# Performance work log

Hardware: AMD Instinct MI355X
Metric: run time of the kernel (lower is better)

The kernel has to match this reference:

```python
import jax, jax.numpy as jnp
import numpy as np

B, T, C = 4, 2048, 768
N_HEADS = 16
HEAD_DIM = C // N_HEADS  # 48
ROPE_BASE = 10000.0


def setup_inputs() -> dict:
    key = jax.random.key(0)
    ks = jax.random.split(key, 6)
    s = 0.02
    return {
        "hidden_states": jax.random.normal(ks[0], (B, T, C), dtype=jnp.float32),
        "attention_mask": jnp.ones((B, T), dtype=jnp.float32),
        "Wq": jax.random.normal(ks[1], (C, C), dtype=jnp.float32) * s,
        "bq": jnp.zeros((C,), dtype=jnp.float32),
        "Wk": jax.random.normal(ks[2], (C, C), dtype=jnp.float32) * s,
        "bk": jnp.zeros((C,), dtype=jnp.float32),
        "Wv": jax.random.normal(ks[3], (C, C), dtype=jnp.float32) * s,
        "bv": jnp.zeros((C,), dtype=jnp.float32),
        "Wo": jax.random.normal(ks[4], (C, C), dtype=jnp.float32) * s,
        "bo": jnp.zeros((C,), dtype=jnp.float32),
    }


def _rotate_half(x):
    x1, x2 = jnp.split(x, 2, axis=-1)
    return jnp.concatenate([-x2, x1], axis=-1)


def reference(hidden_states, attention_mask, Wq, bq, Wk, bk, Wv, bv, Wo, bo):
    b, t, c = hidden_states.shape
    h, d = N_HEADS, c // N_HEADS

    def split_heads(x):  # [b,t,c] -> [b,h,t,d]
        return x.reshape(b, t, h, d).transpose(0, 2, 1, 3)

    q = split_heads(hidden_states @ Wq.T + bq)
    k = split_heads(hidden_states @ Wk.T + bk)
    v = split_heads(hidden_states @ Wv.T + bv)

    # rotary embedding: cos/sin [t, d]
    pos = jnp.arange(t, dtype=jnp.float32)
    inv_freq = 1.0 / (ROPE_BASE ** (jnp.arange(0, d, 2, dtype=jnp.float32) / d))
    freqs = pos[:, None] * inv_freq[None, :]          # [t, d/2]
    emb = jnp.concatenate([freqs, freqs], axis=-1)    # [t, d]
    cos, sin = jnp.cos(emb), jnp.sin(emb)
    q = q * cos + _rotate_half(q) * sin
    k = k * cos + _rotate_half(k) * sin

    scores = jnp.einsum('bhqd,bhkd->bhqk', q, k) / jnp.sqrt(jnp.asarray(d, q.dtype))
    # additive padding mask: (1 - mask) * -10000, broadcast [b,1,1,t]
    scores = scores + (1.0 - attention_mask)[:, None, None, :] * -10000.0
    # causal mask with -inf
    causal = jnp.tril(jnp.ones((t, t), dtype=bool))
    scores = jnp.where(causal[None, None], scores, -jnp.inf)

    probs = jax.nn.softmax(scores, axis=-1)
    ctx = jnp.einsum('bhqk,bhkd->bhqd', probs, v)
    ctx = ctx.transpose(0, 2, 1, 3).reshape(b, t, c)
    return ctx @ Wo.T + bo
```

## Files before the change

kernel.cpp:

```cpp
#include <hip/hip_runtime.h>
#include <hip/hip_bf16.h>
#include <math.h>

#define BB 4
#define TT 2048
#define CC 768
#define NHD 16
#define HD 48
#define NQT 32

typedef __hip_bfloat16 bf16;
typedef __attribute__((ext_vector_type(8))) short short8;
typedef __attribute__((ext_vector_type(4))) float floatx4;

__device__ __forceinline__ unsigned short f2bf(float x) {
    bf16 h = __float2bfloat16(x);
    return *(unsigned short*)&h;
}
__device__ __forceinline__ float bfu2f(unsigned short u) {
    return __uint_as_float(((unsigned)u) << 16);
}

__device__ __forceinline__ void gl_lds16(const void* g, void* s) {
    __builtin_amdgcn_global_load_lds((const __attribute__((address_space(1))) void*)g,
                                     (__attribute__((address_space(3))) void*)s, 16, 0, 0);
}

__device__ __forceinline__ unsigned int pk_bf2(float a, float b) {
    unsigned int ua = __float_as_uint(a) + 0x8000u;
    unsigned int ub = __float_as_uint(b) + 0x8000u;
    return __builtin_amdgcn_perm(ub, ua, 0x07060302);
}

__global__ __launch_bounds__(256) void cast_hs(const float* __restrict__ src,
                                               unsigned short* __restrict__ dst) {
    int i = (blockIdx.x * 256 + threadIdx.x) * 4;
    float4 v = *(const float4*)(src + i);
    ushort4 p;
    p.x = f2bf(v.x); p.y = f2bf(v.y); p.z = f2bf(v.z); p.w = f2bf(v.w);
    *(ushort4*)(dst + i) = p;
}

__global__ __launch_bounds__(256) void cast_w4(const float* __restrict__ s0, const float* __restrict__ s1,
                                               const float* __restrict__ s2, const float* __restrict__ s3,
                                               unsigned short* __restrict__ d0, unsigned short* __restrict__ d1,
                                               unsigned short* __restrict__ d2, unsigned short* __restrict__ d3) {
    const float* s; unsigned short* d;
    switch (blockIdx.y) {
        case 0: s = s0; d = d0; break;
        case 1: s = s1; d = d1; break;
        case 2: s = s2; d = d2; break;
        default: s = s3; d = d3; break;
    }
    int i = (blockIdx.x * 256 + threadIdx.x) * 4;
    float4 v = *(const float4*)(s + i);
    ushort4 p;
    p.x = f2bf(v.x); p.y = f2bf(v.y); p.z = f2bf(v.z); p.w = f2bf(v.w);
    *(ushort4*)(d + i) = p;
}

__global__ __launch_bounds__(256) void rope_table(float2* __restrict__ tab) {
    int idx = blockIdx.x * 256 + threadIdx.x;
    int t = idx / 24, p = idx % 24;
    float inv_freq = powf(10000.0f, -((float)(2 * p) / (float)HD));
    float ang = (float)t * inv_freq;
    float sn, cs;
    sincosf(ang, &sn, &cs);
    tab[idx] = make_float2(cs, sn);
}

template <int MODE>
__global__ __launch_bounds__(256) void gemm_mfma(const unsigned short* __restrict__ A,
                                                 const unsigned short* __restrict__ Bw,
                                                 const float* __restrict__ b0p,
                                                 const float* __restrict__ b1p,
                                                 const float* __restrict__ b2p,
                                                 void* __restrict__ out0,
                                                 void* __restrict__ out1,
                                                 void* __restrict__ out2) {
    __shared__ __align__(16) unsigned short As[128][64];
    __shared__ __align__(16) unsigned short Bs[128][64];
    const int tid = threadIdx.x;
    const int w = tid >> 6, lane = tid & 63;
    const int quad = lane >> 4, ln = lane & 15;
    const int wr = w >> 1, wc = w & 1;

    const int NXB = (MODE == 1) ? 18 : 6;
    const int bx = blockIdx.x;
    const int xcd = bx & 7, slot = bx >> 3;
    const int n0 = (slot % NXB) * 128;
    const int m0 = ((slot / NXB) * 8 + xcd) * 128;

    const int srow = lane >> 3;
    const int ssw = ((lane & 7) ^ srow) * 8;
    const unsigned short* agp[4];
    const unsigned short* bgp[4];
    void* asl[4];
    void* bsl[4];
#pragma unroll
    for (int i = 0; i < 4; ++i) {
        const int R = i * 32 + w * 8;
        agp[i] = A + (size_t)(m0 + R + srow) * CC + ssw;
        bgp[i] = Bw + (size_t)(n0 + R + srow) * CC + ssw;
        asl[i] = &As[R][0];
        bsl[i] = &Bs[R][0];
    }

    floatx4 acc[4][4];
#pragma unroll
    for (int mi = 0; mi < 4; ++mi)
#pragma unroll
        for (int ni = 0; ni < 4; ++ni) acc[mi][ni] = (floatx4){0.f, 0.f, 0.f, 0.f};

    const int ps0 = (quad ^ (ln & 7)) * 8;

    for (int k0 = 0; k0 < CC; k0 += 64) {
        __syncthreads();
#pragma unroll
        for (int i = 0; i < 4; ++i) {
            gl_lds16(agp[i] + k0, asl[i]);
            gl_lds16(bgp[i] + k0, bsl[i]);
        }
        __syncthreads();
#pragma unroll
        for (int kh = 0; kh < 2; ++kh) {
            const int ps = ps0 ^ (kh * 32);
            short8 af[4], bfr[4];
#pragma unroll
            for (int mi = 0; mi < 4; ++mi)
                af[mi] = *(const short8*)&As[wr * 64 + mi * 16 + ln][ps];
#pragma unroll
            for (int ni = 0; ni < 4; ++ni)
                bfr[ni] = *(const short8*)&Bs[wc * 64 + ni * 16 + ln][ps];
#pragma unroll
            for (int mi = 0; mi < 4; ++mi)
#pragma unroll
                for (int ni = 0; ni < 4; ++ni)
                    acc[mi][ni] = __builtin_amdgcn_mfma_f32_16x16x32_bf16(af[mi], bfr[ni], acc[mi][ni], 0, 0, 0);
        }
    }

    if (MODE == 0) {
        float* outf = (float*)out0;
        float bv[4];
#pragma unroll
        for (int ni = 0; ni < 4; ++ni) bv[ni] = b0p[n0 + wc * 64 + ni * 16 + ln];
#pragma unroll
        for (int mi = 0; mi < 4; ++mi)
#pragma unroll
            for (int r = 0; r < 4; ++r) {
                size_t row = m0 + wr * 64 + mi * 16 + quad * 4 + r;
#pragma unroll
                for (int ni = 0; ni < 4; ++ni)
                    outf[row * CC + n0 + wc * 64 + ni * 16 + ln] = acc[mi][ni][r] + bv[ni];
            }
    } else {
        const int seg = n0 / CC;
        const int nl0 = n0 - seg * CC;
        const float* bp = (seg == 0) ? b0p : (seg == 1) ? b1p : b2p;
        float bv[4];
#pragma unroll
        for (int ni = 0; ni < 4; ++ni) bv[ni] = bp[nl0 + wc * 64 + ni * 16 + ln];

        if (seg < 2) {
            unsigned short* outb = (unsigned short*)(seg == 0 ? out0 : out1);
#pragma unroll
            for (int mi = 0; mi < 4; ++mi)
#pragma unroll
                for (int r = 0; r < 4; ++r) {
                    size_t row = m0 + wr * 64 + mi * 16 + quad * 4 + r;
#pragma unroll
                    for (int ni = 0; ni < 4; ++ni)
                        outb[row * CC + nl0 + wc * 64 + ni * 16 + ln] = f2bf(acc[mi][ni][r] + bv[ni]);
                }
        } else {
            unsigned short* outb = (unsigned short*)out2;
            const int b = m0 >> 11;
#pragma unroll
            for (int ni = 0; ni < 4; ++ni) {
                int col = nl0 + wc * 64 + ni * 16 + ln;
                int h = col / HD, d = col % HD;
                size_t base = (size_t)((b * NHD + h) * HD + d) * TT;
#pragma unroll
                for (int mi = 0; mi < 4; ++mi) {
                    int t = (m0 & 2047) + wr * 64 + mi * 16 + quad * 4;
                    ushort4 pk;
                    pk.x = f2bf(acc[mi][ni][0] + bv[ni]);
                    pk.y = f2bf(acc[mi][ni][1] + bv[ni]);
                    pk.z = f2bf(acc[mi][ni][2] + bv[ni]);
                    pk.w = f2bf(acc[mi][ni][3] + bv[ni]);
                    *(ushort4*)(outb + base + t) = pk;
                }
            }
        }
    }
}

__global__ __launch_bounds__(256) void rope_bf(unsigned short* __restrict__ q,
                                               unsigned short* __restrict__ k,
                                               const float2* __restrict__ tab) {
    int idx = blockIdx.x * blockDim.x + threadIdx.x;
    const int HALF = HD / 2;
    int p = idx % HALF;
    int rest = idx / HALF;
    int h = rest % NHD;
    int n = rest / NHD;
    int t = n % TT;
    const float QSC = 0.14433756729740643f * 1.4426950408889634f;
    float2 cssn = tab[t * HALF + p];
    float cs = cssn.x, sn = cssn.y;
    size_t base = (size_t)n * CC + h * HD + p;
    float x1 = bfu2f(q[base]), x2 = bfu2f(q[base + HALF]);
    q[base] = f2bf((x1 * cs - x2 * sn) * QSC);
    q[base + HALF] = f2bf((x2 * cs + x1 * sn) * QSC);
    x1 = bfu2f(k[base]); x2 = bfu2f(k[base + HALF]);
    k[base] = f2bf(x1 * cs - x2 * sn);
    k[base + HALF] = f2bf(x2 * cs + x1 * sn);
}

__global__ __launch_bounds__(256) void attn_kernel(const unsigned short* __restrict__ qb,
                                                   const unsigned short* __restrict__ kb,
                                                   const unsigned short* __restrict__ vt,
                                                   const float* __restrict__ amask,
                                                   unsigned short* __restrict__ ctx) {
    const int bx = blockIdx.x;
    const int xcd = bx & 7;
    const int rem = bx >> 3;
    const int pair = rem & 15;
    const int j = ((rem >> 4) << 3) | xcd;
    const int b = j >> 4, h = j & 15;
    const int tid = threadIdx.x;
    const int w = tid >> 6, lane = tid & 63;
    const int g = lane >> 4, ln = lane & 15;

    __shared__ __align__(16) unsigned short Qs[64][72];
    __shared__ __align__(16) unsigned short Ks[64][72];
    __shared__ __align__(16) unsigned short Vs[64][72];
    __shared__ __align__(16) unsigned short Pw[4][16][72];
    __shared__ __align__(16) float l_s[4][16];

    {
        short8 z8 = {0, 0, 0, 0, 0, 0, 0, 0};
        short8 o8 = {0x3F80, 0, 0, 0, 0, 0, 0, 0};
        short8 ones8 = {0x3F80, 0x3F80, 0x3F80, 0x3F80, 0x3F80, 0x3F80, 0x3F80, 0x3F80};
        if (tid < 128) {
            int r = tid >> 1, half = tid & 1;
            *(short8*)&Qs[r][48 + half * 8] = half ? z8 : o8;
            int t2 = tid;
            *(short8*)&Ks[t2 >> 1][48 + (t2 & 1) * 8] = z8;
        } else if (tid < 128 + 144) {
            int t3 = tid - 128;
            int r = 48 + t3 / 9, cseg = t3 % 9;
            *(short8*)&Vs[r][cseg * 8] = (r == 48) ? ones8 : z8;
        }
    }

    const int ck1 = tid + 256;
    const int rK0 = tid / 6, sK0 = tid % 6;
    const int rK1 = ck1 / 6, sK1 = ck1 % 6;
    const int rV0 = tid >> 3, sV0 = tid & 7;
    const int rV1 = ck1 >> 3, sV1 = ck1 & 7;
    const unsigned short* kbase0 = kb + (size_t)(b * TT + rK0) * CC + h * HD + sK0 * 8;
    const unsigned short* kbase1 = kb + (size_t)(b * TT + rK1) * CC + h * HD + sK1 * 8;
    const unsigned short* vbase0 = vt + (size_t)((b * NHD + h) * HD + rV0) * TT + sV0 * 8;
    const unsigned short* vbase1 = vt + (size_t)((b * NHD + h) * HD + rV1) * TT + sV1 * 8;
    const float* mbase = amask + b * TT + (tid & 63);
    const float MBS = -10000.0f * 1.4426950408889634f;

    for (int rep = 0; rep < 2; ++rep) {
        const int qt = rep ? (NQT - 1 - pair) : pair;
        const int q0 = qt * 64;
        __syncthreads();
        *(short8*)&Qs[rK0][sK0 * 8] =
            *(const short8*)(qb + (size_t)(b * TT + q0 + rK0) * CC + h * HD + sK0 * 8);
        if (tid < 128)
            *(short8*)&Qs[rK1][sK1 * 8] =
                *(const short8*)(qb + (size_t)(b * TT + q0 + rK1) * CC + h * HD + sK1 * 8);

        const unsigned short* kp0 = kbase0;
        const unsigned short* kp1 = kbase1;
        const unsigned short* vp0 = vbase0;
        const unsigned short* vp1 = vbase1;
        const float* mp = mbase;
        short8 kr0, kr1, vr0, vr1;
        float mr = 1.0f;
        kr0 = *(const short8*)kp0;
        vr0 = *(const short8*)vp0;
        if (tid < 128) { kr1 = *(const short8*)kp1; vr1 = *(const short8*)vp1; }
        if (tid < 64) mr = *mp;
        __syncthreads();

        short8 aq0 = *(const short8*)&Qs[w * 16 + ln][g * 8];
        short8 aq1 = *(const short8*)&Qs[w * 16 + ln][32 + g * 8];
        const int q_lane = q0 + w * 16 + ln;

        floatx4 o0 = {0.f, 0.f, 0.f, 0.f}, o1 = o0, o2 = o0, o3 = o0;

        for (int kt = 0; kt <= qt; ++kt) {
            __syncthreads();
            *(short8*)&Ks[rK0][sK0 * 8] = kr0;
            *(short8*)&Vs[rV0][sV0 * 8] = vr0;
            if (tid < 128) {
                *(short8*)&Ks[rK1][sK1 * 8] = kr1;
                *(short8*)&Vs[rV1][sV1 * 8] = vr1;
            }
            if (tid < 64) Ks[tid][48] = f2bf((1.0f - mr) * MBS);
            __syncthreads();

            if (kt < qt) {
                kp0 += (size_t)64 * CC; kr0 = *(const short8*)kp0;
                vp0 += 64;              vr0 = *(const short8*)vp0;
                if (tid < 128) {
                    kp1 += (size_t)64 * CC; kr1 = *(const short8*)kp1;
                    vp1 += 64;              vr1 = *(const short8*)vp1;
                }
                if (tid < 64) { mp += 64; mr = *mp; }
            }

            const int k0 = kt * 64;
            floatx4 sc[4];
#pragma unroll
            for (int c = 0; c < 4; ++c) {
                short8 kf0 = *(const short8*)&Ks[c * 16 + ln][g * 8];
                short8 kf1 = *(const short8*)&Ks[c * 16 + ln][32 + g * 8];
                floatx4 z = {0.f, 0.f, 0.f, 0.f};
                z = __builtin_amdgcn_mfma_f32_16x16x32_bf16(kf0, aq0, z, 0, 0, 0);
                z = __builtin_amdgcn_mfma_f32_16x16x32_bf16(kf1, aq1, z, 0, 0, 0);
                sc[c] = z;
            }

            const bool diag = (kt == qt);
#pragma unroll
            for (int c = 0; c < 4; ++c) {
                float pv[4];
#pragma unroll
                for (int r = 0; r < 4; ++r) {
                    float e = __builtin_amdgcn_exp2f(sc[c][r]);
                    if (diag && (k0 + c * 16 + g * 4 + r > q_lane)) e = 0.f;
                    pv[r] = e;
                }
                uint2 pk;
                pk.x = pk_bf2(pv[0], pv[1]);
                pk.y = pk_bf2(pv[2], pv[3]);
                *(uint2*)&Pw[w][ln][c * 16 + g * 4] = pk;
            }
            short8 pa0 = *(const short8*)&Pw[w][ln][g * 8];
            short8 pa1 = *(const short8*)&Pw[w][ln][32 + g * 8];
#pragma unroll
            for (int n = 0; n < 4; ++n) {
                short8 vb0 = *(const short8*)&Vs[n * 16 + ln][g * 8];
                short8 vb1 = *(const short8*)&Vs[n * 16 + ln][32 + g * 8];
                floatx4 acc = (n == 0) ? o0 : (n == 1) ? o1 : (n == 2) ? o2 : o3;
                acc = __builtin_amdgcn_mfma_f32_16x16x32_bf16(pa0, vb0, acc, 0, 0, 0);
                acc = __builtin_amdgcn_mfma_f32_16x16x32_bf16(pa1, vb1, acc, 0, 0, 0);
                if (n == 0) o0 = acc; else if (n == 1) o1 = acc; else if (n == 2) o2 = acc; else o3 = acc;
            }
        }

        if (ln == 0) *(floatx4*)&l_s[w][g * 4] = o3;
        floatx4 l4 = *(const floatx4*)&l_s[w][g * 4];
#pragma unroll
        for (int r = 0; r < 4; ++r) {
            float inv_l = 1.0f / l4[r];
            int t = q0 + w * 16 + g * 4 + r;
            unsigned short* dst = ctx + (size_t)(b * TT + t) * CC + h * HD;
            dst[ln] = f2bf(o0[r] * inv_l);
            dst[16 + ln] = f2bf(o1[r] * inv_l);
            dst[32 + ln] = f2bf(o2[r] * inv_l);
        }
    }
}

extern "C" void kernel_launch(void* const* d_in, const int* in_sizes, int n_in,
                              void* d_out, int out_size, void* d_ws, size_t ws_size,
                              hipStream_t stream) {
    const float* hs = (const float*)d_in[0];
    const float* amask = (const float*)d_in[1];
    const float* Wq = (const float*)d_in[2];
    const float* bq = (const float*)d_in[3];
    const float* Wk = (const float*)d_in[4];
    const float* bk = (const float*)d_in[5];
    const float* Wv = (const float*)d_in[6];
    const float* bv = (const float*)d_in[7];
    const float* Wo = (const float*)d_in[8];
    const float* bo = (const float*)d_in[9];

    const size_t NELEM = (size_t)BB * TT * CC;
    const size_t WELEM = (size_t)CC * CC;
    unsigned short* hb  = (unsigned short*)d_ws;
    unsigned short* qbuf = hb + NELEM;
    unsigned short* kbuf = qbuf + NELEM;
    unsigned short* vtb = kbuf + NELEM;
    unsigned short* ctxb = vtb + NELEM;
    unsigned short* wqb = ctxb + NELEM;
    unsigned short* wkb = wqb + WELEM;
    unsigned short* wvb = wkb + WELEM;
    unsigned short* wob = wvb + WELEM;
    float2* ropetab = (float2*)(wob + WELEM);

    cast_hs<<<NELEM / 1024, 256, 0, stream>>>(hs, hb);
    dim3 wgrid(WELEM / 1024, 4);
    cast_w4<<<wgrid, 256, 0, stream>>>(Wq, Wk, Wv, Wo, wqb, wkb, wvb, wob);
    rope_table<<<(TT * (HD / 2)) / 256, 256, 0, stream>>>(ropetab);

    gemm_mfma<1><<<18 * 64, 256, 0, stream>>>(hb, wqb, bq, bk, bv, qbuf, kbuf, vtb);

    int rope_total = BB * TT * NHD * (HD / 2);
    rope_bf<<<rope_total / 256, 256, 0, stream>>>(qbuf, kbuf, ropetab);

    attn_kernel<<<1024, 256, 0, stream>>>(qbuf, kbuf, vtb, amask, ctxb);

    gemm_mfma<0><<<6 * 64, 256, 0, stream>>>(ctxb, wob, bo, nullptr, nullptr,
                                             (float*)d_out, nullptr, nullptr);
}
```

Before: 234.6 us.

## Split attention to one Q tile per block, load Q/V straight to registers, vectorize RoPE

Each attention block now handles a single query tile, with tiles interleaved light and heavy, instead of a pair of complementary tiles. The grid doubles to 2048 blocks and occupancy is raised with a launch-bounds hint. Q fragments and V fragments are read directly from global memory into MFMA operand registers, which removes the Q and V shared-memory tiles and their staging. A constant ones vector supplies the row-sum column. RoPE now processes 8 elements per thread with 16-byte vector loads and stores. The risks are more uncoalesced per-lane global V reads inside the loop with no prefetch, and per-block load imbalance across the causal tiles.

New measurement: 394.3 us. 68.0% more time.

```diff
diff --git a/kernel.cpp b/kernel.cpp
--- a/kernel.cpp
+++ b/kernel.cpp
@@ -201,173 +201,171 @@
                                                const float2* __restrict__ tab) {
     int idx = blockIdx.x * blockDim.x + threadIdx.x;
     const int HALF = HD / 2;
-    int p = idx % HALF;
-    int rest = idx / HALF;
+    int p8 = idx % 3;
+    int rest = idx / 3;
     int h = rest % NHD;
     int n = rest / NHD;
-    int t = n % TT;
+    int t = n & (TT - 1);
     const float QSC = 0.14433756729740643f * 1.4426950408889634f;
-    float2 cssn = tab[t * HALF + p];
-    float cs = cssn.x, sn = cssn.y;
-    size_t base = (size_t)n * CC + h * HD + p;
-    float x1 = bfu2f(q[base]), x2 = bfu2f(q[base + HALF]);
-    q[base] = f2bf((x1 * cs - x2 * sn) * QSC);
-    q[base + HALF] = f2bf((x2 * cs + x1 * sn) * QSC);
-    x1 = bfu2f(k[base]); x2 = bfu2f(k[base + HALF]);
-    k[base] = f2bf(x1 * cs - x2 * sn);
-    k[base + HALF] = f2bf(x2 * cs + x1 * sn);
-}
-
-__global__ __launch_bounds__(256) void attn_kernel(const unsigned short* __restrict__ qb,
-                                                   const unsigned short* __restrict__ kb,
-                                                   const unsigned short* __restrict__ vt,
-                                                   const float* __restrict__ amask,
-                                                   unsigned short* __restrict__ ctx) {
+    size_t base = (size_t)n * CC + h * HD + p8 * 8;
+    const float2* tp = tab + t * HALF + p8 * 8;
+
+    short8 q1 = *(const short8*)(q + base);
+    short8 q2 = *(const short8*)(q + base + HALF);
+    short8 k1 = *(const short8*)(k + base);
+    short8 k2 = *(const short8*)(k + base + HALF);
+    short8 r1, r2, s1, s2;
+#pragma unroll
+    for (int jj = 0; jj < 8; ++jj) {
+        float2 cssn = tp[jj];
+        float cs = cssn.x, sn = cssn.y;
+        float a = bfu2f((unsigned short)q1[jj]), bb = bfu2f((unsigned short)q2[jj]);
+        r1[jj] = (short)f2bf((a * cs - bb * sn) * QSC);
+        r2[jj] = (short)f2bf((bb * cs + a * sn) * QSC);
+        float c2 = bfu2f((unsigned short)k1[jj]), d2 = bfu2f((unsigned short)k2[jj]);
+        s1[jj] = (short)f2bf(c2 * cs - d2 * sn);
+        s2[jj] = (short)f2bf(d2 * cs + c2 * sn);
+    }
+    *(short8*)(q + base) = r1;
+    *(short8*)(q + base + HALF) = r2;
+    *(short8*)(k + base) = s1;
+    *(short8*)(k + base + HALF) = s2;
+}
+
+__global__ __launch_bounds__(256, 8) void attn_kernel(const unsigned short* __restrict__ qb,
+                                                      const unsigned short* __restrict__ kb,
+                                                      const unsigned short* __restrict__ vt,
+                                                      const float* __restrict__ amask,
+                                                      unsigned short* __restrict__ ctx) {
     const int bx = blockIdx.x;
     const int xcd = bx & 7;
     const int rem = bx >> 3;
-    const int pair = rem & 15;
-    const int j = ((rem >> 4) << 3) | xcd;
+    const int u = rem & 31;
+    const int qt = (u & 1) ? (31 - (u >> 1)) : (u >> 1);
+    const int j = ((rem >> 5) << 3) | xcd;
     const int b = j >> 4, h = j & 15;
     const int tid = threadIdx.x;
     const int w = tid >> 6, lane = tid & 63;
     const int g = lane >> 4, ln = lane & 15;
 
-    __shared__ __align__(16) unsigned short Qs[64][72];
     __shared__ __align__(16) unsigned short Ks[64][72];
-    __shared__ __align__(16) unsigned short Vs[64][72];
     __shared__ __align__(16) unsigned short Pw[4][16][72];
     __shared__ __align__(16) float l_s[4][16];
 
-    {
-        short8 z8 = {0, 0, 0, 0, 0, 0, 0, 0};
-        short8 o8 = {0x3F80, 0, 0, 0, 0, 0, 0, 0};
-        short8 ones8 = {0x3F80, 0x3F80, 0x3F80, 0x3F80, 0x3F80, 0x3F80, 0x3F80, 0x3F80};
-        if (tid < 128) {
-            int r = tid >> 1, half = tid & 1;
-            *(short8*)&Qs[r][48 + half * 8] = half ? z8 : o8;
-            int t2 = tid;
-            *(short8*)&Ks[t2 >> 1][48 + (t2 & 1) * 8] = z8;
-        } else if (tid < 128 + 144) {
-            int t3 = tid - 128;
-            int r = 48 + t3 / 9, cseg = t3 % 9;
-            *(short8*)&Vs[r][cseg * 8] = (r == 48) ? ones8 : z8;
-        }
+    const short8 z8 = {0, 0, 0, 0, 0, 0, 0, 0};
+    const short8 ones8 = {0x3F80, 0x3F80, 0x3F80, 0x3F80, 0x3F80, 0x3F80, 0x3F80, 0x3F80};
+
+    if (tid < 128) {
+        int r = tid >> 1, half = tid & 1;
+        *(short8*)&Ks[r][48 + half * 8] = z8;
     }
 
     const int ck1 = tid + 256;
     const int rK0 = tid / 6, sK0 = tid % 6;
     const int rK1 = ck1 / 6, sK1 = ck1 % 6;
-    const int rV0 = tid >> 3, sV0 = tid & 7;
-    const int rV1 = ck1 >> 3, sV1 = ck1 & 7;
-    const unsigned short* kbase0 = kb + (size_t)(b * TT + rK0) * CC + h * HD + sK0 * 8;
-    const unsigned short* kbase1 = kb + (size_t)(b * TT + rK1) * CC + h * HD + sK1 * 8;
-    const unsigned short* vbase0 = vt + (size_t)((b * NHD + h) * HD + rV0) * TT + sV0 * 8;
-    const unsigned short* vbase1 = vt + (size_t)((b * NHD + h) * HD + rV1) * TT + sV1 * 8;
-    const float* mbase = amask + b * TT + (tid & 63);
+    const unsigned short* kp0 = kb + (size_t)(b * TT + rK0) * CC + h * HD + sK0 * 8;
+    const unsigned short* kp1 = kb + (size_t)(b * TT + rK1) * CC + h * HD + sK1 * 8;
+    const float* mp = amask + b * TT + (tid & 63);
     const float MBS = -10000.0f * 1.4426950408889634f;
 
-    for (int rep = 0; rep < 2; ++rep) {
-        const int qt = rep ? (NQT - 1 - pair) : pair;
-        const int q0 = qt * 64;
+    const unsigned short* vp0 = vt + ((size_t)((b * NHD + h) * HD) + 0 * 16 + ln) * TT + g * 8;
+    const unsigned short* vp1 = vt + ((size_t)((b * NHD + h) * HD) + 1 * 16 + ln) * TT + g * 8;
+    const unsigned short* vp2 = vt + ((size_t)((b * NHD + h) * HD) + 2 * 16 + ln) * TT + g * 8;
+    const short8 vone = (ln == 0) ? ones8 : z8;
+
+    const int q0 = qt * 64;
+
+    const unsigned short* qrow = qb + (size_t)(b * TT + q0 + w * 16 + ln) * CC + h * HD;
+    short8 aq0 = *(const short8*)(qrow + g * 8);
+    short8 aq1;
+    if (g < 2) {
+        aq1 = *(const short8*)(qrow + 32 + g * 8);
+    } else {
+        aq1 = z8;
+        if (g == 2) aq1[0] = (short)0x3F80;
+    }
+
+    short8 kr0, kr1;
+    float mr = 1.0f;
+    kr0 = *(const short8*)kp0;
+    if (tid < 128) kr1 = *(const short8*)kp1;
+    if (tid < 64) mr = *mp;
+
+    const int q_lane = q0 + w * 16 + ln;
+    floatx4 o0 = {0.f, 0.f, 0.f, 0.f}, o1 = o0, o2 = o0, o3 = o0;
+
+    for (int kt = 0; kt <= qt; ++kt) {
         __syncthreads();
-        *(short8*)&Qs[rK0][sK0 * 8] =
-            *(const short8*)(qb + (size_t)(b * TT + q0 + rK0) * CC + h * HD + sK0 * 8);
-        if (tid < 128)
-            *(short8*)&Qs[rK1][sK1 * 8] =
-                *(const short8*)(qb + (size_t)(b * TT + q0 + rK1) * CC + h * HD + sK1 * 8);
-
-        const unsigned short* kp0 = kbase0;
-        const unsigned short* kp1 = kbase1;
-        const unsigned short* vp0 = vbase0;
-        const unsigned short* vp1 = vbase1;
-        const float* mp = mbase;
-        short8 kr0, kr1, vr0, vr1;
-        float mr = 1.0f;
-        kr0 = *(const short8*)kp0;
-        vr0 = *(const short8*)vp0;
-        if (tid < 128) { kr1 = *(const short8*)kp1; vr1 = *(const short8*)vp1; }
-        if (tid < 64) mr = *mp;
+        *(short8*)&Ks[rK0][sK0 * 8] = kr0;
+        if (tid < 128) *(short8*)&Ks[rK1][sK1 * 8] = kr1;
+        if (tid < 64) Ks[tid][48] = f2bf((1.0f - mr) * MBS);
         __syncthreads();
 
-        short8 aq0 = *(const short8*)&Qs[w * 16 + ln][g * 8];
-        short8 aq1 = *(const short8*)&Qs[w * 16 + ln][32 + g * 8];
-        const int q_lane = q0 + w * 16 + ln;
-
-        floatx4 o0 = {0.f, 0.f, 0.f, 0.f}, o1 = o0, o2 = o0, o3 = o0;
-
-        for (int kt = 0; kt <= qt; ++kt) {
-            __syncthreads();
-            *(short8*)&Ks[rK0][sK0 * 8] = kr0;
-            *(short8*)&Vs[rV0][sV0 * 8] = vr0;
-            if (tid < 128) {
-                *(short8*)&Ks[rK1][sK1 * 8] = kr1;
-                *(short8*)&Vs[rV1][sV1 * 8] = vr1;
+        if (kt < qt) {
+            kp0 += (size_t)64 * CC; kr0 = *(const short8*)kp0;
+            if (tid < 128) { kp1 += (size_t)64 * CC; kr1 = *(const short8*)kp1; }
+            if (tid < 64) { mp += 64; mr = *mp; }
+        }
+
+        const int k0 = kt * 64;
+        floatx4 sc[4];
+#pragma unroll
+        for (int c = 0; c < 4; ++c) {
+            short8 kf0 = *(const short8*)&Ks[c * 16 + ln][g * 8];
+            short8 kf1 = *(const short8*)&Ks[c * 16 + ln][32 + g * 8];
+            floatx4 z = {0.f, 0.f, 0.f, 0.f};
+            z = __builtin_amdgcn_mfma_f32_16x16x32_bf16(kf0, aq0, z, 0, 0, 0);
+            z = __builtin_amdgcn_mfma_f32_16x16x32_bf16(kf1, aq1, z, 0, 0, 0);
+            sc[c] = z;
+        }
+
+        const bool diag = (kt == qt);
+#pragma unroll
+        for (int c = 0; c < 4; ++c) {
+            float pv[4];
+#pragma unroll
+            for (int r = 0; r < 4; ++r) {
+                float e = __builtin_amdgcn_exp2f(sc[c][r]);
+                if (diag && (k0 + c * 16 + g * 4 + r > q_lane)) e = 0.f;
+                pv[r] = e;
             }
-            if (tid < 64) Ks[tid][48] = f2bf((1.0f - mr) * MBS);
-            __syncthreads();
-
-            if (kt < qt) {
-                kp0 += (size_t)64 * CC; kr0 = *(const short8*)kp0;
-                vp0 += 64;              vr0 = *(const short8*)vp0;
-                if (tid < 128) {
-                    kp1 += (size_t)64 * CC; kr1 = *(const short8*)kp1;
-                    vp1 += 64;              vr1 = *(const short8*)vp1;
-                }
-                if (tid < 64) { mp += 64; mr = *mp; }
-            }
-
-            const int k0 = kt * 64;
-            floatx4 sc[4];
-#pragma unroll
-            for (int c = 0; c < 4; ++c) {
-                short8 kf0 = *(const short8*)&Ks[c * 16 + ln][g * 8];
-                short8 kf1 = *(const short8*)&Ks[c * 16 + ln][32 + g * 8];
-                floatx4 z = {0.f, 0.f, 0.f, 0.f};
-                z = __builtin_amdgcn_mfma_f32_16x16x32_bf16(kf0, aq0, z, 0, 0, 0);
-                z = __builtin_amdgcn_mfma_f32_16x16x32_bf16(kf1, aq1, z, 0, 0, 0);
-                sc[c] = z;
-            }
-
-            const bool diag = (kt == qt);
-#pragma unroll
-            for (int c = 0; c < 4; ++c) {
-                float pv[4];
-#pragma unroll
-                for (int r = 0; r < 4; ++r) {
-                    float e = __builtin_amdgcn_exp2f(sc[c][r]);
-                    if (diag && (k0 + c * 16 + g * 4 + r > q_lane)) e = 0.f;
-                    pv[r] = e;
-                }
-                uint2 pk;
-                pk.x = pk_bf2(pv[0], pv[1]);
-                pk.y = pk_bf2(pv[2], pv[3]);
-                *(uint2*)&Pw[w][ln][c * 16 + g * 4] = pk;
-            }
-            short8 pa0 = *(const short8*)&Pw[w][ln][g * 8];
-            short8 pa1 = *(const short8*)&Pw[w][ln][32 + g * 8];
-#pragma unroll
-            for (int n = 0; n < 4; ++n) {
-                short8 vb0 = *(const short8*)&Vs[n * 16 + ln][g * 8];
-                short8 vb1 = *(const short8*)&Vs[n * 16 + ln][32 + g * 8];
-                floatx4 acc = (n == 0) ? o0 : (n == 1) ? o1 : (n == 2) ? o2 : o3;
-                acc = __builtin_amdgcn_mfma_f32_16x16x32_bf16(pa0, vb0, acc, 0, 0, 0);
-                acc = __builtin_amdgcn_mfma_f32_16x16x32_bf16(pa1, vb1, acc, 0, 0, 0);
-                if (n == 0) o0 = acc; else if (n == 1) o1 = acc; else if (n == 2) o2 = acc; else o3 = acc;
-            }
-        }
-
-        if (ln == 0) *(floatx4*)&l_s[w][g * 4] = o3;
-        floatx4 l4 = *(const floatx4*)&l_s[w][g * 4];
-#pragma unroll
-        for (int r = 0; r < 4; ++r) {
-            float inv_l = 1.0f / l4[r];
-            int t = q0 + w * 16 + g * 4 + r;
-            unsigned short* dst = ctx + (size_t)(b * TT + t) * CC + h * HD;
-            dst[ln] = f2bf(o0[r] * inv_l);
-            dst[16 + ln] = f2bf(o1[r] * inv_l);
-            dst[32 + ln] = f2bf(o2[r] * inv_l);
-        }
+            uint2 pk;
+            pk.x = pk_bf2(pv[0], pv[1]);
+            pk.y = pk_bf2(pv[2], pv[3]);
+            *(uint2*)&Pw[w][ln][c * 16 + g * 4] = pk;
+        }
+
+        short8 v00 = *(const short8*)vp0;
+        short8 v01 = *(const short8*)(vp0 + 32);
+        short8 v10 = *(const short8*)vp1;
+        short8 v11 = *(const short8*)(vp1 + 32);
+        short8 v20 = *(const short8*)vp2;
+        short8 v21 = *(const short8*)(vp2 + 32);
+        vp0 += 64; vp1 += 64; vp2 += 64;
+
+        short8 pa0 = *(const short8*)&Pw[w][ln][g * 8];
+        short8 pa1 = *(const short8*)&Pw[w][ln][32 + g * 8];
+
+        o0 = __builtin_amdgcn_mfma_f32_16x16x32_bf16(pa0, v00, o0, 0, 0, 0);
+        o0 = __builtin_amdgcn_mfma_f32_16x16x32_bf16(pa1, v01, o0, 0, 0, 0);
+        o1 = __builtin_amdgcn_mfma_f32_16x16x32_bf16(pa0, v10, o1, 0, 0, 0);
+        o1 = __builtin_amdgcn_mfma_f32_16x16x32_bf16(pa1, v11, o1, 0, 0, 0);
+        o2 = __builtin_amdgcn_mfma_f32_16x16x32_bf16(pa0, v20, o2, 0, 0, 0);
+        o2 = __builtin_amdgcn_mfma_f32_16x16x32_bf16(pa1, v21, o2, 0, 0, 0);
+        o3 = __builtin_amdgcn_mfma_f32_16x16x32_bf16(pa0, vone, o3, 0, 0, 0);
+        o3 = __builtin_amdgcn_mfma_f32_16x16x32_bf16(pa1, vone, o3, 0, 0, 0);
+    }
+
+    if (ln == 0) *(floatx4*)&l_s[w][g * 4] = o3;
+    floatx4 l4 = *(const floatx4*)&l_s[w][g * 4];
+#pragma unroll
+    for (int r = 0; r < 4; ++r) {
+        float inv_l = 1.0f / l4[r];
+        int t = q0 + w * 16 + g * 4 + r;
+        unsigned short* dst = ctx + (size_t)(b * TT + t) * CC + h * HD;
+        dst[ln] = f2bf(o0[r] * inv_l);
+        dst[16 + ln] = f2bf(o1[r] * inv_l);
+        dst[32 + ln] = f2bf(o2[r] * inv_l);
     }
 }
 
@@ -405,10 +403,10 @@
 
     gemm_mfma<1><<<18 * 64, 256, 0, stream>>>(hb, wqb, bq, bk, bv, qbuf, kbuf, vtb);
 
-    int rope_total = BB * TT * NHD * (HD / 2);
+    int rope_total = BB * TT * NHD * 3;
     rope_bf<<<rope_total / 256, 256, 0, stream>>>(qbuf, kbuf, ropetab);
 
-    attn_kernel<<<1024, 256, 0, stream>>>(qbuf, kbuf, vtb, amask, ctxb);
+    attn_kernel<<<2048, 256, 0, stream>>>(qbuf, kbuf, vtb, amask, ctxb);
 
     gemm_mfma<0><<<6 * 64, 256, 0, stream>>>(ctxb, wob, bo, nullptr, nullptr,
                                              (float*)d_out, nullptr, nullptr);
```
